# Performance work log

Measured on AMD Instinct MI355X. Metric: run time of the kernel, lower is better.

Reference implementation:

```python
import jax, jax.numpy as jnp
import numpy as np

B, N, DN, DT = 1024, 200, 128, 128
M = DN + DN + DT  # model_dim = 384 (node + edge + time dims)


def setup_inputs() -> dict:
    key = jax.random.key(0)
    ks = jax.random.split(key, 10)
    rn = lambda k, s, sc=1.0: jax.random.normal(k, s, jnp.float32) * sc
    return {
        'src': rn(ks[0], (B, DN)),
        'src_t': rn(ks[1], (B, 1, DT)),
        'seq': rn(ks[2], (B, N, DN)),
        'seq_t': rn(ks[3], (B, N, DT)),
        'seq_e': rn(ks[4], (B, N, DN)),
        'mask': jax.random.randint(ks[5], (B, N), 0, 2).astype(bool),
        'shared_attn': rn(ks[6], (1, 2 * M), 0.05),
        'fc_w': rn(ks[7], (M, M), 0.05),
        'ln_g': jnp.ones((M,), jnp.float32),
        'ln_b': jnp.zeros((M,), jnp.float32),
        'agg_fc_w1': rn(ks[8], (2 * DN, M + DN), 0.05),
        'agg_fc_w2': rn(ks[9], (DN, 2 * DN), 0.05),
    }


def _layer_norm(x, g, b, eps=1e-5):
    mu = x.mean(-1, keepdims=True)
    var = ((x - mu) ** 2).mean(-1, keepdims=True)
    return (x - mu) * jax.lax.rsqrt(var + eps) * g + b


def reference(src, src_t, seq, seq_t, seq_e, mask, shared_attn, fc_w, ln_g, ln_b, agg_fc_w1, agg_fc_w2):
    # AttnModel.forward with 'simple' Attention (eval mode: dropout off)
    src_ext = src[:, None, :]                                   # [B,1,DN]
    q = jnp.concatenate([src_ext, jnp.zeros_like(src_ext), src_t], axis=2)  # [B,1,M]
    k = jnp.concatenate([seq, seq_e, seq_t], axis=2)            # [B,N,M]
    # F.linear(cat([q_exp, k_exp], -1), shared_attn) == q.w_q + k.w_k (fused, avoids [B,1,N,2M])
    w = shared_attn[0]
    wq, wk = w[:M], w[M:]
    scores = jnp.einsum('bqd,d->bq', q, wq)[:, :, None] + jnp.einsum('bnd,d->bn', k, wk)[:, None, :]  # [B,1,N]
    scores = jnp.where(mask[:, None, :], -1e10, scores)
    attn = jax.nn.softmax(scores, axis=2)                       # [B,1,N]
    out = jnp.einsum('bqn,bnm->bqm', attn, k)                   # [B,1,M] (v == k)
    out = out @ fc_w.T
    out = _layer_norm(out + q, ln_g, ln_b)
    out = out[:, 0, :]                                          # [B,M]
    attn_w = attn[:, 0, :]                                      # [B,N]
    x = jnp.concatenate([out, src], axis=1)                     # [B, M+DN]
    x = jax.nn.relu(x @ agg_fc_w1.T)                            # [B, 2*DN]
    out = x @ agg_fc_w2.T                                       # [B, DN]
    return out, attn_w
```

## Files before the change

### kernel.cpp

```cpp
#include <hip/hip_runtime.h>


constexpr int B_   = 1024;
constexpr int N_   = 200;
constexpr int DN_  = 128;
constexpr int DT_  = 128;
constexpr int M_   = 384;
constexpr int BDIM = 1024;
constexpr int ROWS = 2;
constexpr int WPR  = 8;
constexpr int NPW  = N_ / WPR;
constexpr int ITER = (NPW + 1) / 2;

__device__ float g_fcT[M_ * M_];
__device__ float g_w1T[(M_ + DN_) * (2 * DN_)];
__device__ float g_w2T[(2 * DN_) * DN_];

__device__ __forceinline__ float half_sum(float v) {
#pragma unroll
    for (int off = 16; off > 0; off >>= 1) v += __shfl_xor(v, off, 64);
    return v;
}
__device__ __forceinline__ float wave_sum(float v) {
#pragma unroll
    for (int off = 32; off > 0; off >>= 1) v += __shfl_xor(v, off, 64);
    return v;
}

__global__ void transpose_weights(const float* __restrict__ fc_w,
                                  const float* __restrict__ w1,
                                  const float* __restrict__ w2) {
    const int stride = gridDim.x * blockDim.x;
    for (int idx = blockIdx.x * blockDim.x + threadIdx.x; idx < M_ * M_; idx += stride) {
        const int j = idx / M_, i = idx - j * M_;
        g_fcT[idx] = fc_w[i * M_ + j];
    }
    for (int idx = blockIdx.x * blockDim.x + threadIdx.x; idx < (M_ + DN_) * (2 * DN_); idx += stride) {
        const int j = idx >> 8, i = idx & 255;
        g_w1T[idx] = w1[i * (M_ + DN_) + j];
    }
    for (int idx = blockIdx.x * blockDim.x + threadIdx.x; idx < (2 * DN_) * DN_; idx += stride) {
        const int j = idx >> 7, i = idx & 127;
        g_w2T[idx] = w2[i * (2 * DN_) + j];
    }
}

__global__ __launch_bounds__(BDIM)
void tgnn_kernel(
    const float* __restrict__ src,
    const float* __restrict__ src_t,
    const float* __restrict__ seq,
    const float* __restrict__ seq_t,
    const float* __restrict__ seq_e,
    const int*   __restrict__ mask,
    const float* __restrict__ shared_attn,
    const float* __restrict__ ln_g,
    const float* __restrict__ ln_b,
    float* __restrict__ out,
    float* __restrict__ attn_out)
{
    const int blk  = blockIdx.x;
    const int tid  = threadIdx.x;
    const int wave = tid >> 6;
    const int lane = tid & 63;
    const int row  = wave >> 3;
    const int wir  = wave & 7;
    const int b    = blk * ROWS + row;
    const int half = lane >> 5;
    const int sub  = lane & 31;
    const int c0   = 4 * sub;

    __shared__ float s_p[ROWS][N_];
    __shared__ float s_q[ROWS][M_];
    __shared__ float s_oa[16][M_];
    __shared__ float s_x[ROWS][M_];
    __shared__ float s_y[ROWS][M_ + DN_];
    __shared__ float s_h[ROWS][2 * DN_];
    __shared__ int   s_mask[ROWS][N_];
    __shared__ float s_red[ROWS][16];
    __shared__ float s_w1p[2][ROWS][256];
    __shared__ float s_w2p[4][ROWS][128];

    for (int idx = tid; idx < ROWS * M_; idx += BDIM) {
        const int r = idx / M_, d = idx - r * M_;
        const int bb = blk * ROWS + r;
        float v = (d < DN_) ? src[bb * DN_ + d]
                            : (d < 2 * DN_ ? 0.0f : src_t[bb * DT_ + (d - 2 * DN_)]);
        s_q[r][d] = v;
    }
    for (int idx = tid; idx < ROWS * N_; idx += BDIM) {
        const int r = idx / N_, n = idx - r * N_;
        s_mask[r][n] = mask[(blk * ROWS + r) * N_ + n];
    }

    const float* wq = shared_attn;
    const float* wk = shared_attn + M_;
    const float4 wkA = *(const float4*)&wk[c0];
    const float4 wkE = *(const float4*)&wk[DN_ + c0];
    const float4 wkT = *(const float4*)&wk[2 * DN_ + c0];
    const float4 wqA = *(const float4*)&wq[c0];
    const float4 wqT = *(const float4*)&wq[2 * DN_ + c0];

    __syncthreads();

    const float4 qa = *(const float4*)&s_q[row][c0];
    const float4 qt = *(const float4*)&s_q[row][2 * DN_ + c0];
    float qp = qa.x * wqA.x + qa.y * wqA.y + qa.z * wqA.z + qa.w * wqA.w
             + qt.x * wqT.x + qt.y * wqT.y + qt.z * wqT.z + qt.w * wqT.w;
    const float qdot = half_sum(qp);

    const int kbase = wir * NPW;
    const float* baseA = seq   + (long)b * (N_ * DN_);
    const float* baseE = seq_e + (long)b * (N_ * DN_);
    const float* baseT = seq_t + (long)b * (N_ * DT_);

    float4 oA = make_float4(0.f, 0.f, 0.f, 0.f);
    float4 oE = oA, oT = oA;
    float lsum = 0.f;

    int iters = ITER;
    asm volatile("" : "+s"(iters));
#pragma unroll 1
    for (int it = 0; it < iters; ++it) {
        const int  ko    = 2 * it + half;
        const bool valid = ko < NPW;
        const int  n     = kbase + (valid ? ko : NPW - 1);
        const int  off   = n * DN_ + c0;
        const float4 a = *(const float4*)(baseA + off);
        const float4 e = *(const float4*)(baseE + off);
        const float4 t = *(const float4*)(baseT + off);
        float part = a.x * wkA.x + a.y * wkA.y + a.z * wkA.z + a.w * wkA.w
                   + e.x * wkE.x + e.y * wkE.y + e.z * wkE.z + e.w * wkE.w
                   + t.x * wkT.x + t.y * wkT.y + t.z * wkT.z + t.w * wkT.w;
        part = half_sum(part);
        const float p = (valid && !s_mask[row][n]) ? __expf(part + qdot) : 0.0f;
        if (sub == 0 && valid) s_p[row][n] = p;
        lsum += p;
        oA.x += p * a.x; oA.y += p * a.y; oA.z += p * a.z; oA.w += p * a.w;
        oE.x += p * e.x; oE.y += p * e.y; oE.z += p * e.z; oE.w += p * e.w;
        oT.x += p * t.x; oT.y += p * t.y; oT.z += p * t.z; oT.w += p * t.w;
    }

    oA.x += __shfl_xor(oA.x, 32, 64); oA.y += __shfl_xor(oA.y, 32, 64);
    oA.z += __shfl_xor(oA.z, 32, 64); oA.w += __shfl_xor(oA.w, 32, 64);
    oE.x += __shfl_xor(oE.x, 32, 64); oE.y += __shfl_xor(oE.y, 32, 64);
    oE.z += __shfl_xor(oE.z, 32, 64); oE.w += __shfl_xor(oE.w, 32, 64);
    oT.x += __shfl_xor(oT.x, 32, 64); oT.y += __shfl_xor(oT.y, 32, 64);
    oT.z += __shfl_xor(oT.z, 32, 64); oT.w += __shfl_xor(oT.w, 32, 64);
    lsum += __shfl_xor(lsum, 32, 64);
    if (lane == 0) s_red[row][wir] = lsum;
    if (half == 0) {
        *(float4*)&s_oa[wave][c0]            = oA;
        *(float4*)&s_oa[wave][DN_ + c0]      = oE;
        *(float4*)&s_oa[wave][2 * DN_ + c0]  = oT;
    }
    __syncthreads();

    for (int idx = tid; idx < ROWS * M_; idx += BDIM) {
        const int r = idx / M_, d = idx - r * M_;
        const float Z = s_red[r][0] + s_red[r][1] + s_red[r][2] + s_red[r][3]
                      + s_red[r][4] + s_red[r][5] + s_red[r][6] + s_red[r][7];
        const float invZ = 1.0f / Z;
        float acc = 0.f;
#pragma unroll
        for (int w = 0; w < 8; ++w) acc += s_oa[8 * r + w][d];
        s_x[r][d] = acc * invZ;
    }
    __syncthreads();

    if (tid < M_) {
        float acc0 = 0.f, acc1 = 0.f;
#pragma unroll 8
        for (int j = 0; j < M_; ++j) {
            const float w = g_fcT[j * M_ + tid];
            acc0 += s_x[0][j] * w;
            acc1 += s_x[1][j] * w;
        }
        s_y[0][tid] = acc0 + s_q[0][tid];
        s_y[1][tid] = acc1 + s_q[1][tid];
    } else if (tid < M_ + 256) {
        const int t2 = tid - M_;
        for (int idx = t2; idx < ROWS * N_; idx += 256) {
            const int r = idx / N_, nn = idx - r * N_;
            const float Z = s_red[r][0] + s_red[r][1] + s_red[r][2] + s_red[r][3]
                          + s_red[r][4] + s_red[r][5] + s_red[r][6] + s_red[r][7];
            attn_out[(blk * ROWS + r) * N_ + nn] = s_p[r][nn] * (1.0f / Z);
        }
    }
    __syncthreads();

    {
        float ls = 0.f, lq = 0.f;
        for (int j = 64 * wir + lane; j < M_; j += 512) {
            const float v = s_y[row][j];
            ls += v; lq += v * v;
        }
        ls = wave_sum(ls); lq = wave_sum(lq);
        if (lane == 0) { s_red[row][wir] = ls; s_red[row][8 + wir] = lq; }
    }
    __syncthreads();
    for (int idx = tid; idx < ROWS * M_; idx += BDIM) {
        const int r = idx / M_, j = idx - r * M_;
        float sm = 0.f, sq2 = 0.f;
#pragma unroll
        for (int w = 0; w < 8; ++w) { sm += s_red[r][w]; sq2 += s_red[r][8 + w]; }
        const float mean = sm * (1.0f / M_);
        const float msq  = sq2 * (1.0f / M_);
        const float rstd = rsqrtf(msq - mean * mean + 1e-5f);
        s_y[r][j] = (s_y[r][j] - mean) * rstd * ln_g[j] + ln_b[j];
    }
    for (int idx = tid; idx < ROWS * DN_; idx += BDIM) {
        const int r = idx >> 7, d = idx & 127;
        s_y[r][M_ + d] = s_q[r][d];
    }
    __syncthreads();

    if (tid < 512) {
        const int kk = tid >> 8, i = tid & 255;
        const int j0 = kk * 256;
        float acc0 = 0.f, acc1 = 0.f;
#pragma unroll 8
        for (int j = j0; j < j0 + 256; ++j) {
            const float w = g_w1T[j * 256 + i];
            acc0 += s_y[0][j] * w;
            acc1 += s_y[1][j] * w;
        }
        s_w1p[kk][0][i] = acc0;
        s_w1p[kk][1][i] = acc1;
    }
    __syncthreads();
    if (tid < 512) {
        const int r = tid >> 8, i = tid & 255;
        s_h[r][i] = fmaxf(s_w1p[0][r][i] + s_w1p[1][r][i], 0.0f);
    }
    __syncthreads();

    if (tid < 512) {
        const int kk = tid >> 7, i = tid & 127;
        const int j0 = kk * 64;
        float acc0 = 0.f, acc1 = 0.f;
#pragma unroll 8
        for (int j = j0; j < j0 + 64; ++j) {
            const float w = g_w2T[j * 128 + i];
            acc0 += s_h[0][j] * w;
            acc1 += s_h[1][j] * w;
        }
        s_w2p[kk][0][i] = acc0;
        s_w2p[kk][1][i] = acc1;
    }
    __syncthreads();
    if (tid < 256) {
        const int r = tid >> 7, i = tid & 127;
        out[(blk * ROWS + r) * DN_ + i] =
            s_w2p[0][r][i] + s_w2p[1][r][i] + s_w2p[2][r][i] + s_w2p[3][r][i];
    }
}

extern "C" void kernel_launch(void* const* d_in, const int* in_sizes, int n_in,
                              void* d_out, int out_size, void* d_ws, size_t ws_size,
                              hipStream_t stream) {
    const float* src         = (const float*)d_in[0];
    const float* src_t       = (const float*)d_in[1];
    const float* seq         = (const float*)d_in[2];
    const float* seq_t       = (const float*)d_in[3];
    const float* seq_e       = (const float*)d_in[4];
    const int*   mask        = (const int*)  d_in[5];
    const float* shared_attn = (const float*)d_in[6];
    const float* fc_w        = (const float*)d_in[7];
    const float* ln_g        = (const float*)d_in[8];
    const float* ln_b        = (const float*)d_in[9];
    const float* w1          = (const float*)d_in[10];
    const float* w2          = (const float*)d_in[11];

    float* outp     = (float*)d_out;
    float* attn_out = (float*)d_out + B_ * DN_;

    transpose_weights<<<256, 256, 0, stream>>>(fc_w, w1, w2);
    tgnn_kernel<<<B_ / ROWS, BDIM, 0, stream>>>(src, src_t, seq, seq_t, seq_e, mask,
                                                shared_attn, ln_g, ln_b, outp, attn_out);
}
```

Before: 356.5 us.

## Prefetch next attention row and split MLP matvecs across all threads

The attention loop now software-pipelines its global loads, fetching the next key row's float4s while the current row is processed, to hide memory latency. The fc, w1 and w2 matrix-vector products are split along the reduction dimension across more threads (768/1024/1024 instead of 384/512/512), with extra shared-memory partial sums and a reduction step. The attn_out write moves before the fc stage. This adds registers, shared memory and an extra sync in exchange for more parallelism in the tail stages.

```diff
diff --git a/kernel.cpp b/kernel.cpp
--- a/kernel.cpp
+++ b/kernel.cpp
@@ -78,8 +78,9 @@
     __shared__ float s_h[ROWS][2 * DN_];
     __shared__ int   s_mask[ROWS][N_];
     __shared__ float s_red[ROWS][16];
-    __shared__ float s_w1p[2][ROWS][256];
-    __shared__ float s_w2p[4][ROWS][128];
+    __shared__ float s_fcp[2][ROWS][M_];
+    __shared__ float s_w1p[4][ROWS][256];
+    __shared__ float s_w2p[8][ROWS][128];
 
     for (int idx = tid; idx < ROWS * M_; idx += BDIM) {
         const int r = idx / M_, d = idx - r * M_;
@@ -118,27 +119,38 @@
     float4 oE = oA, oT = oA;
     float lsum = 0.f;
 
-    int iters = ITER;
-    asm volatile("" : "+s"(iters));
+    {
+        const int off0 = (kbase + half) * DN_ + c0;
+        float4 a = *(const float4*)(baseA + off0);
+        float4 e = *(const float4*)(baseE + off0);
+        float4 t = *(const float4*)(baseT + off0);
+
+        int iters = ITER;
+        asm volatile("" : "+s"(iters));
 #pragma unroll 1
-    for (int it = 0; it < iters; ++it) {
-        const int  ko    = 2 * it + half;
-        const bool valid = ko < NPW;
-        const int  n     = kbase + (valid ? ko : NPW - 1);
-        const int  off   = n * DN_ + c0;
-        const float4 a = *(const float4*)(baseA + off);
-        const float4 e = *(const float4*)(baseE + off);
-        const float4 t = *(const float4*)(baseT + off);
-        float part = a.x * wkA.x + a.y * wkA.y + a.z * wkA.z + a.w * wkA.w
-                   + e.x * wkE.x + e.y * wkE.y + e.z * wkE.z + e.w * wkE.w
-                   + t.x * wkT.x + t.y * wkT.y + t.z * wkT.z + t.w * wkT.w;
-        part = half_sum(part);
-        const float p = (valid && !s_mask[row][n]) ? __expf(part + qdot) : 0.0f;
-        if (sub == 0 && valid) s_p[row][n] = p;
-        lsum += p;
-        oA.x += p * a.x; oA.y += p * a.y; oA.z += p * a.z; oA.w += p * a.w;
-        oE.x += p * e.x; oE.y += p * e.y; oE.z += p * e.z; oE.w += p * e.w;
-        oT.x += p * t.x; oT.y += p * t.y; oT.z += p * t.z; oT.w += p * t.w;
+        for (int it = 0; it < iters; ++it) {
+            const int  ko_c  = 2 * it + half;
+            const bool val_c = ko_c < NPW;
+            const int  n_c   = kbase + (val_c ? ko_c : NPW - 1);
+            const int  itn   = (it + 1 < ITER) ? it + 1 : it;
+            const int  ko_n  = 2 * itn + half;
+            const int  n_n   = kbase + ((ko_n < NPW) ? ko_n : NPW - 1);
+            const int  off_n = n_n * DN_ + c0;
+            const float4 an = *(const float4*)(baseA + off_n);
+            const float4 en = *(const float4*)(baseE + off_n);
+            const float4 tn = *(const float4*)(baseT + off_n);
+            float part = a.x * wkA.x + a.y * wkA.y + a.z * wkA.z + a.w * wkA.w
+                       + e.x * wkE.x + e.y * wkE.y + e.z * wkE.z + e.w * wkE.w
+                       + t.x * wkT.x + t.y * wkT.y + t.z * wkT.z + t.w * wkT.w;
+            part = half_sum(part);
+            const float p = (val_c && !s_mask[row][n_c]) ? __expf(part + qdot) : 0.0f;
+            if (sub == 0 && val_c) s_p[row][n_c] = p;
+            lsum += p;
+            oA.x += p * a.x; oA.y += p * a.y; oA.z += p * a.z; oA.w += p * a.w;
+            oE.x += p * e.x; oE.y += p * e.y; oE.z += p * e.z; oE.w += p * e.w;
+            oT.x += p * t.x; oT.y += p * t.y; oT.z += p * t.z; oT.w += p * t.w;
+            a = an; e = en; t = tn;
+        }
     }
 
     oA.x += __shfl_xor(oA.x, 32, 64); oA.y += __shfl_xor(oA.y, 32, 64);
@@ -166,26 +178,32 @@
         for (int w = 0; w < 8; ++w) acc += s_oa[8 * r + w][d];
         s_x[r][d] = acc * invZ;
     }
-    __syncthreads();
-
-    if (tid < M_) {
+    for (int idx = tid; idx < ROWS * N_; idx += BDIM) {
+        const int r = idx / N_, nn = idx - r * N_;
+        const float Z = s_red[r][0] + s_red[r][1] + s_red[r][2] + s_red[r][3]
+                      + s_red[r][4] + s_red[r][5] + s_red[r][6] + s_red[r][7];
+        attn_out[(blk * ROWS + r) * N_ + nn] = s_p[r][nn] * (1.0f / Z);
+    }
+    __syncthreads();
+
+    if (tid < 2 * M_) {
+        const int kk = (tid >= M_) ? 1 : 0;
+        const int i  = tid - kk * M_;
+        const int j0 = kk * (M_ / 2);
         float acc0 = 0.f, acc1 = 0.f;
-#pragma unroll 8
-        for (int j = 0; j < M_; ++j) {
-            const float w = g_fcT[j * M_ + tid];
+#pragma unroll 16
+        for (int j = j0; j < j0 + M_ / 2; ++j) {
+            const float w = g_fcT[j * M_ + i];
             acc0 += s_x[0][j] * w;
             acc1 += s_x[1][j] * w;
         }
-        s_y[0][tid] = acc0 + s_q[0][tid];
-        s_y[1][tid] = acc1 + s_q[1][tid];
-    } else if (tid < M_ + 256) {
-        const int t2 = tid - M_;
-        for (int idx = t2; idx < ROWS * N_; idx += 256) {
-            const int r = idx / N_, nn = idx - r * N_;
-            const float Z = s_red[r][0] + s_red[r][1] + s_red[r][2] + s_red[r][3]
-                          + s_red[r][4] + s_red[r][5] + s_red[r][6] + s_red[r][7];
-            attn_out[(blk * ROWS + r) * N_ + nn] = s_p[r][nn] * (1.0f / Z);
-        }
+        s_fcp[kk][0][i] = acc0;
+        s_fcp[kk][1][i] = acc1;
+    }
+    __syncthreads();
+    for (int idx = tid; idx < ROWS * M_; idx += BDIM) {
+        const int r = idx / M_, i = idx - r * M_;
+        s_y[r][i] = s_fcp[0][r][i] + s_fcp[1][r][i] + s_q[r][i];
     }
     __syncthreads();
 
@@ -215,12 +233,12 @@
     }
     __syncthreads();
 
-    if (tid < 512) {
+    {
         const int kk = tid >> 8, i = tid & 255;
-        const int j0 = kk * 256;
+        const int j0 = kk * 128;
         float acc0 = 0.f, acc1 = 0.f;
-#pragma unroll 8
-        for (int j = j0; j < j0 + 256; ++j) {
+#pragma unroll 16
+        for (int j = j0; j < j0 + 128; ++j) {
             const float w = g_w1T[j * 256 + i];
             acc0 += s_y[0][j] * w;
             acc1 += s_y[1][j] * w;
@@ -231,16 +249,17 @@
     __syncthreads();
     if (tid < 512) {
         const int r = tid >> 8, i = tid & 255;
-        s_h[r][i] = fmaxf(s_w1p[0][r][i] + s_w1p[1][r][i], 0.0f);
-    }
-    __syncthreads();
-
-    if (tid < 512) {
+        s_h[r][i] = fmaxf(s_w1p[0][r][i] + s_w1p[1][r][i] +
+                          s_w1p[2][r][i] + s_w1p[3][r][i], 0.0f);
+    }
+    __syncthreads();
+
+    {
         const int kk = tid >> 7, i = tid & 127;
-        const int j0 = kk * 64;
+        const int j0 = kk * 32;
         float acc0 = 0.f, acc1 = 0.f;
-#pragma unroll 8
-        for (int j = j0; j < j0 + 64; ++j) {
+#pragma unroll 16
+        for (int j = j0; j < j0 + 32; ++j) {
             const float w = g_w2T[j * 128 + i];
             acc0 += s_h[0][j] * w;
             acc1 += s_h[1][j] * w;
@@ -251,8 +270,10 @@
     __syncthreads();
     if (tid < 256) {
         const int r = tid >> 7, i = tid & 127;
-        out[(blk * ROWS + r) * DN_ + i] =
-            s_w2p[0][r][i] + s_w2p[1][r][i] + s_w2p[2][r][i] + s_w2p[3][r][i];
+        float v = 0.f;
+#pragma unroll
+        for (int kk = 0; kk < 8; ++kk) v += s_w2p[kk][r][i];
+        out[(blk * ROWS + r) * DN_ + i] = v;
     }
 }
 
```

New measurement: 341.1 us. -4.3%, faster.
